# Kernel tuning notes

Hardware: AMD Instinct MI355X
Metric: run time of the kernel (lower is better)

Reference implementation:

```python
import jax, jax.numpy as jnp
import numpy as np

ITERS = 3

def squash(s, axis):
    # v = (|s|^2 / (1 + |s|^2)) * s / |s|
    sn = jnp.sum(s * s, axis=axis, keepdims=True)
    return sn / (1.0 + sn) * s / jnp.sqrt(sn)

def setup_inputs() -> dict:
    key = jax.random.key(0)
    k1, k2 = jax.random.split(key)
    b, B, C, P2, f = 8, 144, 16, 16, 12
    u = jax.random.normal(k1, (b, B, C, P2, f, f), dtype=jnp.float32)
    a = jax.random.uniform(k2, (b, B, f, f), dtype=jnp.float32)
    return {"u": u, "a": a}

def reference(u, a):
    # u: (b, B, C, P2, f, f); a: (b, B, f, f)
    b, B, C, P2, f, _ = u.shape
    # r: (b, B, C, 1, f, f), initialized uniform over C scaled by activation
    r = jnp.broadcast_to(a[:, :, None, None, :, :] * (1.0 / C), (b, B, C, 1, f, f))
    v = None
    for i in range(ITERS):
        c = jax.nn.softmax(r, axis=2)                       # over C
        v = squash(jnp.sum(c * u, axis=1, keepdims=True), axis=3)  # (b,1,C,P2,f,f)
        if i != ITERS - 1:
            r = r + jnp.sum(u * v, axis=3, keepdims=True)   # agreement over psize
    a_out = jnp.sqrt(jnp.sum(v * v, axis=3, keepdims=True))  # (b,1,C,1,f,f)
    return (jnp.squeeze(v, axis=1), jnp.squeeze(a_out, axis=(1, 3)))
```

## Files before the change

### kernel.cpp

```cpp
#include <hip/hip_runtime.h>
#include <math.h>


#define NB 8
#define BDIM 144
#define CDIM 16
#define PDIM 16
#define SDIM 144
#define PLANE (PDIM * SDIM)
#define VELEMS (NB * CDIM * PLANE)
#define AELEMS (NB * CDIM * SDIM)
#define NCHUNK 9

__device__ __forceinline__ float4 ld4(const float* p) { return *(const float4*)p; }
__device__ __forceinline__ void st4(float* p, float4 v) { *(float4*)p = v; }

template <int CTRL>
__device__ __forceinline__ float dpp_mov(float x) {
  return __int_as_float(__builtin_amdgcn_update_dpp(
      0, __float_as_int(x), CTRL, 0xF, 0xF, true));
}
__device__ __forceinline__ float rowsum16(float x) {
  x += dpp_mov<0xB1>(x);
  x += dpp_mov<0x4E>(x);
  x += dpp_mov<0x124>(x);
  x += dpp_mov<0x128>(x);
  return x;
}

__global__ __launch_bounds__(256, 2) void s_pass(const float* __restrict__ u,
                                                 const float* __restrict__ a,
                                                 const float* __restrict__ V,
                                                 float* __restrict__ spart,
                                                 int it) {
  __shared__ float4 red[3 * 64 * 17];
  const int lane = threadIdx.x & 63;
  const int w = threadIdx.x >> 6;
  const int c = lane & 15;
  const int posq = lane >> 4;
  const int b = blockIdx.z;
  const int pos0 = blockIdx.y * 16 + posq * 4;
  const int B0 = blockIdx.x * 16 + w * 4;

  const float* ub =
      u + ((size_t)((b * BDIM + B0) * CDIM + c) * PDIM) * SDIM + pos0;

  float4 Vt[16];
  if (it) {
    const float* vb = V + ((size_t)(b * CDIM + c) * PDIM) * SDIM + pos0;
#pragma unroll
    for (int p = 0; p < 16; ++p) Vt[p] = ld4(vb + p * SDIM);
  }

  float4 sacc[16];
#pragma unroll
  for (int p = 0; p < 16; ++p) sacc[p] = make_float4(0.f, 0.f, 0.f, 0.f);

#pragma unroll 1
  for (int j = 0; j < 4; ++j) {
    const float* uj = ub + (size_t)j * (CDIM * PLANE);
    float4 uv[16];
#pragma unroll
    for (int p = 0; p < 16; ++p) uv[p] = ld4(uj + p * SDIM);

    float4 wt;
    if (it) {
      float4 d = make_float4(0.f, 0.f, 0.f, 0.f);
#pragma unroll
      for (int p = 0; p < 16; ++p) {
        d.x += uv[p].x * Vt[p].x; d.y += uv[p].y * Vt[p].y;
        d.z += uv[p].z * Vt[p].z; d.w += uv[p].w * Vt[p].w;
      }
      const float4 a4 = ld4(a + (size_t)(b * BDIM + B0 + j) * SDIM + pos0);
      float4 e;
      e.x = __expf(fmaf(a4.x, 0.0625f, d.x));
      e.y = __expf(fmaf(a4.y, 0.0625f, d.y));
      e.z = __expf(fmaf(a4.z, 0.0625f, d.z));
      e.w = __expf(fmaf(a4.w, 0.0625f, d.w));
      wt.x = e.x * __builtin_amdgcn_rcpf(rowsum16(e.x));
      wt.y = e.y * __builtin_amdgcn_rcpf(rowsum16(e.y));
      wt.z = e.z * __builtin_amdgcn_rcpf(rowsum16(e.z));
      wt.w = e.w * __builtin_amdgcn_rcpf(rowsum16(e.w));
    } else {
      wt = make_float4(0.0625f, 0.0625f, 0.0625f, 0.0625f);
    }
#pragma unroll
    for (int p = 0; p < 16; ++p) {
      sacc[p].x += wt.x * uv[p].x; sacc[p].y += wt.y * uv[p].y;
      sacc[p].z += wt.z * uv[p].z; sacc[p].w += wt.w * uv[p].w;
    }
  }

  if (w > 0) {
    float4* dst = &red[(w - 1) * 64 * 17 + lane * 17];
#pragma unroll
    for (int p = 0; p < 16; ++p) dst[p] = sacc[p];
  }
  __syncthreads();
  if (w == 0) {
#pragma unroll 1
    for (int k = 0; k < 3; ++k) {
      const float4* src = &red[k * 64 * 17 + lane * 17];
#pragma unroll
      for (int p = 0; p < 16; ++p) {
        const float4 x = src[p];
        sacc[p].x += x.x; sacc[p].y += x.y; sacc[p].z += x.z; sacc[p].w += x.w;
      }
    }
    float* sp = spart + (size_t)blockIdx.x * VELEMS +
                ((size_t)(b * CDIM + c) * PDIM) * SDIM + pos0;
#pragma unroll
    for (int p = 0; p < 16; ++p) st4(sp + p * SDIM, sacc[p]);
  }
}

__global__ __launch_bounds__(256) void q_kernel(const float* __restrict__ spart,
                                                float* __restrict__ V,
                                                float* __restrict__ out_v,
                                                float* __restrict__ out_a,
                                                int it) {
  const int gid = blockIdx.x * 256 + threadIdx.x;
  const int pos = gid % SDIM;
  const int bc = gid / SDIM;
  const size_t base = (size_t)bc * PLANE + pos;

  float sv[16];
  float sn = 0.f;
#pragma unroll
  for (int p = 0; p < 16; ++p) {
    float x = spart[base + p * SDIM];
#pragma unroll
    for (int k = 1; k < NCHUNK; ++k)
      x += spart[(size_t)k * VELEMS + base + p * SDIM];
    sv[p] = x;
    sn += x * x;
  }
  const float g = sn * __builtin_amdgcn_rcpf(1.f + sn);
  const float sc = g * rsqrtf(sn);

  if (it == 0) {
#pragma unroll
    for (int p = 0; p < 16; ++p) V[base + p * SDIM] = sv[p] * sc;
  } else if (it == 1) {
#pragma unroll
    for (int p = 0; p < 16; ++p) V[base + p * SDIM] += sv[p] * sc;
  } else {
#pragma unroll
    for (int p = 0; p < 16; ++p) out_v[base + p * SDIM] = sv[p] * sc;
    out_a[gid] = g;
  }
}

extern "C" void kernel_launch(void* const* d_in, const int* in_sizes, int n_in,
                              void* d_out, int out_size, void* d_ws, size_t ws_size,
                              hipStream_t stream) {
  const float* u = (const float*)d_in[0];
  const float* a = (const float*)d_in[1];
  float* V = (float*)d_ws;
  float* spart = V + VELEMS;
  float* out_v = (float*)d_out;
  float* out_a = out_v + VELEMS;

  const dim3 gS(NCHUNK, 9, NB);
  for (int it = 0; it < 3; ++it) {
    s_pass<<<gS, 256, 0, stream>>>(u, a, V, spart, it);
    q_kernel<<<AELEMS / 256, 256, 0, stream>>>(spart, V, out_v, out_a, it);
  }
}
```

Baseline: 382.5 us.

## Split routing pass into separate logit, softmax and weighted-sum kernels

Replaces the fused per-iteration s_pass with separate stages. p0_kernel does the uniform first sum, d_kernel computes agreement logits, w_kernel does the exp and softmax denominator over C, and a_kernel does the weighted accumulation. The partial-sum chunk count rises from 9 to 36, which removes the shared-memory block reduction and raises occupancy, and q_kernel switches to 64-thread blocks. The trade is more launches, reading u twice per later iteration instead of once, and extra global traffic for the logits buffer and the larger partial-sum buffer.

```diff
diff --git a/kernel.cpp b/kernel.cpp
--- a/kernel.cpp
+++ b/kernel.cpp
@@ -10,143 +10,165 @@
 #define PLANE (PDIM * SDIM)
 #define VELEMS (NB * CDIM * PLANE)
 #define AELEMS (NB * CDIM * SDIM)
-#define NCHUNK 9
+#define RELEMS (NB * BDIM * CDIM * SDIM)
+#define DENELEMS (NB * BDIM * SDIM)
+#define NCHUNK 36
+#define BSTRIDE (CDIM * PLANE)
 
 __device__ __forceinline__ float4 ld4(const float* p) { return *(const float4*)p; }
 __device__ __forceinline__ void st4(float* p, float4 v) { *(float4*)p = v; }
 
-template <int CTRL>
-__device__ __forceinline__ float dpp_mov(float x) {
-  return __int_as_float(__builtin_amdgcn_update_dpp(
-      0, __float_as_int(x), CTRL, 0xF, 0xF, true));
-}
-__device__ __forceinline__ float rowsum16(float x) {
-  x += dpp_mov<0xB1>(x);
-  x += dpp_mov<0x4E>(x);
-  x += dpp_mov<0x124>(x);
-  x += dpp_mov<0x128>(x);
-  return x;
-}
-
-__global__ __launch_bounds__(256, 2) void s_pass(const float* __restrict__ u,
-                                                 const float* __restrict__ a,
-                                                 const float* __restrict__ V,
-                                                 float* __restrict__ spart,
-                                                 int it) {
-  __shared__ float4 red[3 * 64 * 17];
-  const int lane = threadIdx.x & 63;
+__global__ __launch_bounds__(256, 4) void p0_kernel(const float* __restrict__ u,
+                                                    float* __restrict__ spart) {
+  const int l = threadIdx.x & 63;
   const int w = threadIdx.x >> 6;
-  const int c = lane & 15;
-  const int posq = lane >> 4;
+  const int c = blockIdx.y, b = blockIdx.z;
+  const int B0 = blockIdx.x * 16 + w * 4;
+  const float* pb = u + (size_t)((b * BDIM + B0) * CDIM + c) * PLANE + 4 * l;
+
+  float4 sacc[9];
+#pragma unroll
+  for (int k = 0; k < 9; ++k) sacc[k] = make_float4(0.f, 0.f, 0.f, 0.f);
+#pragma unroll 1
+  for (int j = 0; j < 4; ++j) {
+    const float* pj = pb + (size_t)j * BSTRIDE;
+#pragma unroll
+    for (int k = 0; k < 9; ++k) {
+      const float4 x = ld4(pj + 256 * k);
+      sacc[k].x += x.x; sacc[k].y += x.y; sacc[k].z += x.z; sacc[k].w += x.w;
+    }
+  }
+  float* sp = spart + (size_t)(blockIdx.x * 4 + w) * VELEMS +
+              (size_t)(b * CDIM + c) * PLANE + 4 * l;
+#pragma unroll
+  for (int k = 0; k < 9; ++k) st4(sp + 256 * k, sacc[k]);
+}
+
+__global__ __launch_bounds__(256, 4) void d_kernel(const float* __restrict__ u,
+                                                   const float* __restrict__ a,
+                                                   const float* __restrict__ V,
+                                                   float* __restrict__ R) {
+  const int l = threadIdx.x & 63;
+  const int w = threadIdx.x >> 6;
+  const int c = l & 15;
+  const int posq = l >> 4;
+  const int b = blockIdx.z;
+  const int pos0 = blockIdx.y * 16 + posq * 4;
+  const int B = blockIdx.x * 4 + w;
+
+  const float* ub = u + ((size_t)((b * BDIM + B) * CDIM + c) * PDIM) * SDIM + pos0;
+  const float* vb = V + ((size_t)(b * CDIM + c) * PDIM) * SDIM + pos0;
+
+  float4 d = make_float4(0.f, 0.f, 0.f, 0.f);
+#pragma unroll
+  for (int p = 0; p < PDIM; ++p) {
+    const float4 uv = ld4(ub + p * SDIM);
+    const float4 vt = ld4(vb + p * SDIM);
+    d.x += uv.x * vt.x; d.y += uv.y * vt.y;
+    d.z += uv.z * vt.z; d.w += uv.w * vt.w;
+  }
+  const float4 a4 = ld4(a + (size_t)(b * BDIM + B) * SDIM + pos0);
+  float4 lg;
+  lg.x = fmaf(a4.x, 0.0625f, d.x); lg.y = fmaf(a4.y, 0.0625f, d.y);
+  lg.z = fmaf(a4.z, 0.0625f, d.z); lg.w = fmaf(a4.w, 0.0625f, d.w);
+  st4(R + (size_t)((b * BDIM + B) * CDIM + c) * SDIM + pos0, lg);
+}
+
+__global__ __launch_bounds__(256) void w_kernel(float* __restrict__ R,
+                                                float* __restrict__ rden) {
+  const int gid = blockIdx.x * 256 + threadIdx.x;
+  const int pos = gid % SDIM;
+  const int bB = gid / SDIM;
+  float* rb = R + (size_t)bB * (CDIM * SDIM) + pos;
+  float e[CDIM];
+  float sum = 0.f;
+#pragma unroll
+  for (int c = 0; c < CDIM; ++c) {
+    e[c] = __expf(rb[c * SDIM]);
+    sum += e[c];
+  }
+#pragma unroll
+  for (int c = 0; c < CDIM; ++c) rb[c * SDIM] = e[c];
+  rden[gid] = 1.0f / sum;
+}
+
+__global__ __launch_bounds__(256, 4) void a_kernel(const float* __restrict__ u,
+                                                   const float* __restrict__ R,
+                                                   const float* __restrict__ rden,
+                                                   float* __restrict__ spart) {
+  const int l = threadIdx.x & 63;
+  const int w = threadIdx.x >> 6;
+  const int c = l & 15;
+  const int posq = l >> 4;
   const int b = blockIdx.z;
   const int pos0 = blockIdx.y * 16 + posq * 4;
   const int B0 = blockIdx.x * 16 + w * 4;
 
-  const float* ub =
-      u + ((size_t)((b * BDIM + B0) * CDIM + c) * PDIM) * SDIM + pos0;
-
-  float4 Vt[16];
-  if (it) {
-    const float* vb = V + ((size_t)(b * CDIM + c) * PDIM) * SDIM + pos0;
-#pragma unroll
-    for (int p = 0; p < 16; ++p) Vt[p] = ld4(vb + p * SDIM);
-  }
-
-  float4 sacc[16];
-#pragma unroll
-  for (int p = 0; p < 16; ++p) sacc[p] = make_float4(0.f, 0.f, 0.f, 0.f);
+  const float* ub = u + ((size_t)((b * BDIM + B0) * CDIM + c) * PDIM) * SDIM + pos0;
+
+  float4 sacc[PDIM];
+#pragma unroll
+  for (int p = 0; p < PDIM; ++p) sacc[p] = make_float4(0.f, 0.f, 0.f, 0.f);
 
 #pragma unroll 1
   for (int j = 0; j < 4; ++j) {
-    const float* uj = ub + (size_t)j * (CDIM * PLANE);
-    float4 uv[16];
-#pragma unroll
-    for (int p = 0; p < 16; ++p) uv[p] = ld4(uj + p * SDIM);
-
+    const int B = B0 + j;
+    const float4 e4 = ld4(R + (size_t)((b * BDIM + B) * CDIM + c) * SDIM + pos0);
+    const float4 r4 = ld4(rden + (size_t)(b * BDIM + B) * SDIM + pos0);
     float4 wt;
-    if (it) {
-      float4 d = make_float4(0.f, 0.f, 0.f, 0.f);
-#pragma unroll
-      for (int p = 0; p < 16; ++p) {
-        d.x += uv[p].x * Vt[p].x; d.y += uv[p].y * Vt[p].y;
-        d.z += uv[p].z * Vt[p].z; d.w += uv[p].w * Vt[p].w;
-      }
-      const float4 a4 = ld4(a + (size_t)(b * BDIM + B0 + j) * SDIM + pos0);
-      float4 e;
-      e.x = __expf(fmaf(a4.x, 0.0625f, d.x));
-      e.y = __expf(fmaf(a4.y, 0.0625f, d.y));
-      e.z = __expf(fmaf(a4.z, 0.0625f, d.z));
-      e.w = __expf(fmaf(a4.w, 0.0625f, d.w));
-      wt.x = e.x * __builtin_amdgcn_rcpf(rowsum16(e.x));
-      wt.y = e.y * __builtin_amdgcn_rcpf(rowsum16(e.y));
-      wt.z = e.z * __builtin_amdgcn_rcpf(rowsum16(e.z));
-      wt.w = e.w * __builtin_amdgcn_rcpf(rowsum16(e.w));
-    } else {
-      wt = make_float4(0.0625f, 0.0625f, 0.0625f, 0.0625f);
+    wt.x = e4.x * r4.x; wt.y = e4.y * r4.y;
+    wt.z = e4.z * r4.z; wt.w = e4.w * r4.w;
+    const float* uj = ub + (size_t)j * BSTRIDE;
+#pragma unroll
+    for (int p = 0; p < PDIM; ++p) {
+      const float4 uv = ld4(uj + p * SDIM);
+      sacc[p].x += wt.x * uv.x; sacc[p].y += wt.y * uv.y;
+      sacc[p].z += wt.z * uv.z; sacc[p].w += wt.w * uv.w;
     }
-#pragma unroll
-    for (int p = 0; p < 16; ++p) {
-      sacc[p].x += wt.x * uv[p].x; sacc[p].y += wt.y * uv[p].y;
-      sacc[p].z += wt.z * uv[p].z; sacc[p].w += wt.w * uv[p].w;
-    }
-  }
-
-  if (w > 0) {
-    float4* dst = &red[(w - 1) * 64 * 17 + lane * 17];
-#pragma unroll
-    for (int p = 0; p < 16; ++p) dst[p] = sacc[p];
-  }
-  __syncthreads();
-  if (w == 0) {
-#pragma unroll 1
-    for (int k = 0; k < 3; ++k) {
-      const float4* src = &red[k * 64 * 17 + lane * 17];
-#pragma unroll
-      for (int p = 0; p < 16; ++p) {
-        const float4 x = src[p];
-        sacc[p].x += x.x; sacc[p].y += x.y; sacc[p].z += x.z; sacc[p].w += x.w;
-      }
-    }
-    float* sp = spart + (size_t)blockIdx.x * VELEMS +
-                ((size_t)(b * CDIM + c) * PDIM) * SDIM + pos0;
-#pragma unroll
-    for (int p = 0; p < 16; ++p) st4(sp + p * SDIM, sacc[p]);
-  }
-}
-
-__global__ __launch_bounds__(256) void q_kernel(const float* __restrict__ spart,
-                                                float* __restrict__ V,
-                                                float* __restrict__ out_v,
-                                                float* __restrict__ out_a,
-                                                int it) {
-  const int gid = blockIdx.x * 256 + threadIdx.x;
+  }
+  float* sp = spart + (size_t)(blockIdx.x * 4 + w) * VELEMS +
+              ((size_t)(b * CDIM + c) * PDIM) * SDIM + pos0;
+#pragma unroll
+  for (int p = 0; p < PDIM; ++p) st4(sp + p * SDIM, sacc[p]);
+}
+
+__global__ __launch_bounds__(64) void q_kernel(const float* __restrict__ spart,
+                                               float* __restrict__ V,
+                                               float* __restrict__ out_v,
+                                               float* __restrict__ out_a,
+                                               float scale, int mode) {
+  const int gid = blockIdx.x * 64 + threadIdx.x;
   const int pos = gid % SDIM;
   const int bc = gid / SDIM;
   const size_t base = (size_t)bc * PLANE + pos;
 
-  float sv[16];
+  float sv[PDIM];
+#pragma unroll
+  for (int p = 0; p < PDIM; ++p) sv[p] = 0.f;
+#pragma unroll 1
+  for (int k = 0; k < NCHUNK; ++k) {
+    const float* sp = spart + (size_t)k * VELEMS + base;
+#pragma unroll
+    for (int p = 0; p < PDIM; ++p) sv[p] += sp[p * SDIM];
+  }
   float sn = 0.f;
 #pragma unroll
-  for (int p = 0; p < 16; ++p) {
-    float x = spart[base + p * SDIM];
-#pragma unroll
-    for (int k = 1; k < NCHUNK; ++k)
-      x += spart[(size_t)k * VELEMS + base + p * SDIM];
-    sv[p] = x;
-    sn += x * x;
+  for (int p = 0; p < PDIM; ++p) {
+    sv[p] *= scale;
+    sn += sv[p] * sv[p];
   }
   const float g = sn * __builtin_amdgcn_rcpf(1.f + sn);
   const float sc = g * rsqrtf(sn);
 
-  if (it == 0) {
-#pragma unroll
-    for (int p = 0; p < 16; ++p) V[base + p * SDIM] = sv[p] * sc;
-  } else if (it == 1) {
-#pragma unroll
-    for (int p = 0; p < 16; ++p) V[base + p * SDIM] += sv[p] * sc;
+  if (mode == 0) {
+#pragma unroll
+    for (int p = 0; p < PDIM; ++p) V[base + p * SDIM] = sv[p] * sc;
+  } else if (mode == 1) {
+#pragma unroll
+    for (int p = 0; p < PDIM; ++p) V[base + p * SDIM] += sv[p] * sc;
   } else {
 #pragma unroll
-    for (int p = 0; p < 16; ++p) out_v[base + p * SDIM] = sv[p] * sc;
+    for (int p = 0; p < PDIM; ++p) out_v[base + p * SDIM] = sv[p] * sc;
     out_a[gid] = g;
   }
 }
@@ -158,12 +180,25 @@
   const float* a = (const float*)d_in[1];
   float* V = (float*)d_ws;
   float* spart = V + VELEMS;
+  float* R = spart + (size_t)NCHUNK * VELEMS;
+  float* rden = R + RELEMS;
   float* out_v = (float*)d_out;
   float* out_a = out_v + VELEMS;
 
-  const dim3 gS(NCHUNK, 9, NB);
-  for (int it = 0; it < 3; ++it) {
-    s_pass<<<gS, 256, 0, stream>>>(u, a, V, spart, it);
-    q_kernel<<<AELEMS / 256, 256, 0, stream>>>(spart, V, out_v, out_a, it);
-  }
-}
+  const dim3 gP0(9, CDIM, NB);
+  const dim3 gD(36, 9, NB);
+  const dim3 gA(9, 9, NB);
+  const int gW = DENELEMS / 256;
+  const int gQ = AELEMS / 64;
+
+  p0_kernel<<<gP0, 256, 0, stream>>>(u, spart);
+  q_kernel<<<gQ, 64, 0, stream>>>(spart, V, out_v, out_a, 0.0625f, 0);
+  d_kernel<<<gD, 256, 0, stream>>>(u, a, V, R);
+  w_kernel<<<gW, 256, 0, stream>>>(R, rden);
+  a_kernel<<<gA, 256, 0, stream>>>(u, R, rden, spart);
+  q_kernel<<<gQ, 64, 0, stream>>>(spart, V, out_v, out_a, 1.0f, 1);
+  d_kernel<<<gD, 256, 0, stream>>>(u, a, V, R);
+  w_kernel<<<gW, 256, 0, stream>>>(R, rden);
+  a_kernel<<<gA, 256, 0, stream>>>(u, R, rden, spart);
+  q_kernel<<<gQ, 64, 0, stream>>>(spart, V, out_v, out_a, 1.0f, 2);
+}
```

Result: slower. 514.0 us (+34.4%).
